# Optimization experiments

Hardware: AMD Instinct MI355X
Metric: run time of the kernel (lower is better)

Reference implementation:

```python
import jax, jax.numpy as jnp
import numpy as np

# ---- module configuration (from init_kwargs) ----
NX, NV = 2048, 1024
LX = 1.0
VMAX = 6.0
DX = LX / NX
DV = 2.0 * VMAX / NV
XS = jnp.linspace(-LX / 2 + DX / 2, LX / 2 - DX / 2, NX)
VS = jnp.linspace(-VMAX + DV / 2, VMAX - DV / 2, NV)
AE, AI = 1.0, 1836.0
ZE, ZI = -1.0, 1.0
OMEGA_C_TAU = 1.0
NU_EE, NU_II = 1.0, 0.1
DT = 1e-3
T_LBO = 1.0  # LBO temperature, u = 0


def minmod(a, b):
    return jnp.where(a * b > 0, jnp.sign(a) * jnp.minimum(jnp.abs(a), jnp.abs(b)), 0.0)


def _sl(a, lo, hi, axis):
    return jax.lax.slice_in_dim(a, lo, hi, axis=axis)


def slope_limited_flux_divergence(f_pad, F, dx, axis):
    # f_pad has N+4 cells along `axis` (2 ghost cells per side). MUSCL + minmod.
    n = f_pad.shape[axis]
    d = _sl(f_pad, 1, n, axis) - _sl(f_pad, 0, n - 1, axis)          # n-1 diffs
    sigma = minmod(_sl(d, 0, n - 2, axis), _sl(d, 1, n - 1, axis))    # slopes for cells 1..n-2
    fc = _sl(f_pad, 1, n - 1, axis)                                   # cells 1..n-2
    m = n - 2
    fL = _sl(fc, 0, m - 1, axis) + 0.5 * _sl(sigma, 0, m - 1, axis)   # left interface states
    fR = _sl(fc, 1, m, axis) - 0.5 * _sl(sigma, 1, m, axis)           # right interface states
    flux = F(fL, fR)                                                  # N+1 interface fluxes
    k = flux.shape[axis]
    return (_sl(flux, 1, k, axis) - _sl(flux, 0, k - 1, axis)) / dx   # N cells


def pad_x_periodic(f):
    return jnp.concatenate([f[-2:, :], f, f[:2, :]], axis=0)


def pad_v_zero(f):
    z = jnp.zeros((f.shape[0], 2), f.dtype)
    return jnp.concatenate([z, f, z], axis=1)


def poisson_solve(rho_c):
    # dE/dx = rho_c, zero-mean E (periodic-compatible gauge)
    E = jnp.cumsum(rho_c) * DX
    return E - jnp.mean(E)


def species_rhs(f, E, A, Z):
    v = VS[None, :]
    Fx = lambda l, r: jnp.where(v > 0, l * v, r * v)                  # upwind in x
    vdfdx = slope_limited_flux_divergence(pad_x_periodic(f), Fx, DX, axis=0)
    Ec = (OMEGA_C_TAU * Z / A) * E[:, None]
    Fv = lambda l, r: jnp.where(Ec > 0, l * Ec, r * Ec)               # upwind in v
    Edfdv = slope_limited_flux_divergence(pad_v_zero(f), Fv, DV, axis=1)
    return -vdfdx - Edfdv


def vlasov_rhs(fe, fi):
    ne = jnp.sum(fe, axis=1) * DV
    ni = jnp.sum(fi, axis=1) * DV
    E = poisson_solve(ZE * ne + ZI * ni)
    return species_rhs(fe, E, AE, ZE), species_rhs(fi, E, AI, ZI)


def ssprk2(fe, fi, dt):
    re, ri = vlasov_rhs(fe, fi)
    fe1, fi1 = fe + dt * re, fi + dt * ri
    re1, ri1 = vlasov_rhs(fe1, fi1)
    return 0.5 * (fe + fe1 + dt * re1), 0.5 * (fi + fi1 + dt * ri1)


def lbo_diagonals(lam):
    # L f = lam * d/dv( v f + T df/dv ), central differences
    vm = jnp.roll(VS, 1)
    vp = jnp.roll(VS, -1)
    dl = lam * (T_LBO / DV**2 - vm / (2 * DV))
    du = lam * (T_LBO / DV**2 + vp / (2 * DV))
    d = lam * (-2.0 * T_LBO / DV**2) * jnp.ones(NV, XS.dtype)
    return dl.at[0].set(0.0), d, du.at[-1].set(0.0)


def nu_shape():
    midpt = LX / 3
    ef = LX / 6 / 10
    h0 = lambda x: 1 + jnp.exp(x / ef - midpt / ef)
    return 1.0 / (0.5 * (h0(XS) + h0(-XS)))  # [Nx]


def thomas(dl, d, du, b):
    # Thomas algorithm; dl[0]==0 and du[-1]==0 assumed.
    def fwd(carry, inp):
        cp, bp = carry
        dli, di, dui, bi = inp
        m = di - dli * cp
        cpi = dui / m
        bpi = (bi - dli * bp) / m
        return (cpi, bpi), (cpi, bpi)
    z = jnp.zeros((), b.dtype)
    _, (cp, bp) = jax.lax.scan(fwd, (z, z), (dl, d, du, b))
    def bwd(x_next, inp):
        cpi, bpi = inp
        x = bpi - cpi * x_next
        return x, x
    _, x = jax.lax.scan(bwd, z, (cp, bp), reverse=True)
    return x


def implicit_collide(f, lam, dt):
    dl, d, du = lbo_diagonals(lam)
    nu = nu_shape()
    def solve_row(nui, frow):
        return thomas(-dt * nui * dl, 1.0 - dt * nui * d, -dt * nui * du, frow)
    return jax.vmap(solve_row)(nu, f)


def setup_inputs() -> dict:
    key = jax.random.key(0)
    k1, k2 = jax.random.split(key)
    fe = jax.random.uniform(k1, (NX, NV), dtype=jnp.float32)
    fi = jax.random.uniform(k2, (NX, NV), dtype=jnp.float32)
    return {"fe": fe, "fi": fi}


def reference(fe, fi):
    fe1, fi1 = ssprk2(fe, fi, DT)
    fe2 = implicit_collide(fe1, NU_EE, DT)
    fi2 = implicit_collide(fi1, NU_II, DT)
    return jnp.stack([fe2, fi2])  # [2, Nx, Nv]
```

## Files before the change

### kernel.cpp

```cpp
#include <hip/hip_runtime.h>
#include <math.h>

#define NX 2048
#define NV 1024
static constexpr float DXf   = 1.0f / 2048.0f;
static constexpr float DVf   = 12.0f / 1024.0f;
static constexpr float DTf   = 0.001f;
static constexpr float INV_DX = 2048.0f;
static constexpr float INV_DV = 1024.0f / 12.0f;

__device__ __forceinline__ float minmod_f(float a, float b) {
    return (a * b > 0.0f) ? (a > 0.0f ? fminf(a, b) : fmaxf(a, b)) : 0.0f;
}

__device__ __forceinline__ float frcp(float x) {
    float r = __builtin_amdgcn_rcpf(x);
    return r * (2.0f - x * r);
}

__device__ __forceinline__ void rhs4(const float* __restrict__ g, int i, int j0, float Ec,
                                     float4& f0v, float4& rv) {
    const float* rowc = g + i * NV;
    const float* rm1  = g + (((i - 1) & (NX - 1)) * NV);
    const float* rm2  = g + (((i - 2) & (NX - 1)) * NV);
    const float* rp1  = g + (((i + 1) & (NX - 1)) * NV);
    const float* rp2  = g + (((i + 2) & (NX - 1)) * NV);

    float4 c   = *(const float4*)(rowc + j0);
    float4 xm1 = *(const float4*)(rm1 + j0);
    float4 xm2 = *(const float4*)(rm2 + j0);
    float4 xp1 = *(const float4*)(rp1 + j0);
    float4 xp2 = *(const float4*)(rp2 + j0);
    float4 lm = make_float4(0.f, 0.f, 0.f, 0.f);
    float4 rp = make_float4(0.f, 0.f, 0.f, 0.f);
    if (j0 >= 4)      lm = *(const float4*)(rowc + j0 - 4);
    if (j0 <= NV - 8) rp = *(const float4*)(rowc + j0 + 4);

    float vals[8] = {lm.z, lm.w, c.x, c.y, c.z, c.w, rp.x, rp.y};
    const float* cc   = (const float*)&c;
    const float* am1  = (const float*)&xm1;
    const float* am2  = (const float*)&xm2;
    const float* ap1  = (const float*)&xp1;
    const float* ap2  = (const float*)&xp2;
    float* f0o = (float*)&f0v;
    float* ro  = (float*)&rv;

    #pragma unroll
    for (int k = 0; k < 4; ++k) {
        float f0  = cc[k];
        float fm1 = am1[k], fm2 = am2[k], fp1 = ap1[k], fp2 = ap2[k];

        float v = DVf * ((float)(j0 + k) + 0.5f) - 6.0f;
        float dm1 = fm1 - fm2, d0 = f0 - fm1, dp1 = fp1 - f0, dp2 = fp2 - fp1;
        float sm1 = minmod_f(dm1, d0);
        float s0  = minmod_f(d0, dp1);
        float sp1 = minmod_f(dp1, dp2);
        float PhiM, PhiP;
        if (v > 0.0f) {
            PhiM = (fm1 + 0.5f * sm1) * v;
            PhiP = (f0  + 0.5f * s0 ) * v;
        } else {
            PhiM = (f0  - 0.5f * s0 ) * v;
            PhiP = (fp1 - 0.5f * sp1) * v;
        }
        float vdfdx = (PhiP - PhiM) * INV_DX;

        float gm2 = vals[k], gm1 = vals[k + 1], gp1 = vals[k + 3], gp2 = vals[k + 4];
        float em1 = gm1 - gm2, e0 = f0 - gm1, ep1 = gp1 - f0, ep2 = gp2 - gp1;
        float tm1 = minmod_f(em1, e0);
        float t0  = minmod_f(e0, ep1);
        float tp1 = minmod_f(ep1, ep2);
        float GM, GP;
        if (Ec > 0.0f) {
            GM = (gm1 + 0.5f * tm1) * Ec;
            GP = (f0  + 0.5f * t0 ) * Ec;
        } else {
            GM = (f0  - 0.5f * t0 ) * Ec;
            GP = (gp1 - 0.5f * tp1) * Ec;
        }
        float Edfdv = (GP - GM) * INV_DV;

        f0o[k] = f0;
        ro[k]  = -vdfdx - Edfdv;
    }
}

__device__ __forceinline__ float compute_E(const float* __restrict__ se,
                                           const float* __restrict__ si, int i) {
    int t = threadIdx.x;
    float pref = 0.0f, wtot = 0.0f;
    #pragma unroll
    for (int q = 0; q < NX / 256; ++q) {
        int k = q * 256 + t;
        float rho = DVf * (si[k] - se[k]);
        if (k <= i) pref += rho;
        wtot += rho * (float)(NX - k);
    }
    #pragma unroll
    for (int off = 32; off > 0; off >>= 1) {
        pref += __shfl_down(pref, off, 64);
        wtot += __shfl_down(wtot, off, 64);
    }
    __shared__ float sp_[4], sw_[4];
    int lane = t & 63, wave = t >> 6;
    if (lane == 0) { sp_[wave] = pref; sw_[wave] = wtot; }
    __syncthreads();
    float P = sp_[0] + sp_[1] + sp_[2] + sp_[3];
    float W = sw_[0] + sw_[1] + sw_[2] + sw_[3];
    return DXf * (P - W * (1.0f / (float)NX));
}

__global__ __launch_bounds__(256) void moments_kernel(const float* __restrict__ fe,
                                                      const float* __restrict__ fi,
                                                      float* __restrict__ se,
                                                      float* __restrict__ si) {
    int i = blockIdx.x;
    int t = threadIdx.x;
    float4 a4 = *(const float4*)(fe + (size_t)i * NV + 4 * t);
    float4 b4 = *(const float4*)(fi + (size_t)i * NV + 4 * t);
    float a = a4.x + a4.y + a4.z + a4.w;
    float b = b4.x + b4.y + b4.z + b4.w;
    __shared__ float r1[4], r2[4];
    #pragma unroll
    for (int off = 32; off > 0; off >>= 1) {
        a += __shfl_down(a, off, 64);
        b += __shfl_down(b, off, 64);
    }
    int lane = t & 63, wave = t >> 6;
    if (lane == 0) { r1[wave] = a; r2[wave] = b; }
    __syncthreads();
    if (t == 0) {
        se[i] = r1[0] + r1[1] + r1[2] + r1[3];
        si[i] = r2[0] + r2[1] + r2[2] + r2[3];
    }
}

__global__ __launch_bounds__(256) void stage1_kernel(const float* __restrict__ fe,
                                                     const float* __restrict__ fi,
                                                     const float* __restrict__ se,
                                                     const float* __restrict__ si,
                                                     float* __restrict__ fe1,
                                                     float* __restrict__ fi1,
                                                     float* __restrict__ se1,
                                                     float* __restrict__ si1) {
    int i  = blockIdx.x;
    int sp = blockIdx.y;
    const float* g = sp ? fi : fe;
    float* out = sp ? fi1 : fe1;
    float zoa = sp ? (1.0f / 1836.0f) : -1.0f;
    float Ec = zoa * compute_E(se, si, i);
    int t = threadIdx.x;
    int j0 = 4 * t;

    float4 f0v, rv;
    rhs4(g, i, j0, Ec, f0v, rv);
    float4 o;
    o.x = f0v.x + DTf * rv.x;
    o.y = f0v.y + DTf * rv.y;
    o.z = f0v.z + DTf * rv.z;
    o.w = f0v.w + DTf * rv.w;
    *(float4*)(out + i * NV + j0) = o;

    float x = o.x + o.y + o.z + o.w;
    #pragma unroll
    for (int off = 32; off > 0; off >>= 1) x += __shfl_down(x, off, 64);
    __shared__ float sred[4];
    int lane = t & 63, wave = t >> 6;
    if (lane == 0) sred[wave] = x;
    __syncthreads();
    if (t == 0) { (sp ? si1 : se1)[i] = sred[0] + sred[1] + sred[2] + sred[3]; }
}

__global__ __launch_bounds__(256) void stage2_collide_kernel(const float* __restrict__ fe,
                                                             const float* __restrict__ fi,
                                                             const float* __restrict__ fe1,
                                                             const float* __restrict__ fi1,
                                                             const float* __restrict__ se1,
                                                             const float* __restrict__ si1,
                                                             float* __restrict__ out) {
    const float Tdv2   = 1.0f / (DVf * DVf);
    const float inv2dv = 0.5f / DVf;

    int i  = blockIdx.x;
    int sp = blockIdx.y;
    const float* h = sp ? fi : fe;
    const float* g = sp ? fi1 : fe1;
    float* orow = out + ((size_t)sp * NX + i) * NV;
    float zoa = sp ? (1.0f / 1836.0f) : -1.0f;
    float lam = sp ? 0.1f : 1.0f;
    float Ec = zoa * compute_E(se1, si1, i);
    int t = threadIdx.x;
    int lane = t & 63;
    int wave = t >> 6;

    __shared__ float lds_f[NV + NV / 16];

    {
        int j0 = 4 * t;
        float4 f0v, rv;
        rhs4(g, i, j0, Ec, f0v, rv);
        float4 h4 = *(const float4*)(h + i * NV + j0);
        int a = j0 + (j0 >> 4);
        lds_f[a]     = 0.5f * h4.x + 0.5f * f0v.x + (0.5f * DTf) * rv.x;
        lds_f[a + 1] = 0.5f * h4.y + 0.5f * f0v.y + (0.5f * DTf) * rv.y;
        lds_f[a + 2] = 0.5f * h4.z + 0.5f * f0v.z + (0.5f * DTf) * rv.z;
        lds_f[a + 3] = 0.5f * h4.w + 0.5f * f0v.w + (0.5f * DTf) * rv.w;
    }
    __syncthreads();
    if (wave != 0) return;

    float xi = DXf * ((float)i + 0.5f) - 0.5f;
    float nu = 1.0f / (1.0f + 0.5f * (expf(60.0f * xi - 20.0f) + expf(-60.0f * xi - 20.0f)));
    float K = DTf * nu * lam;
    float b = 1.0f + 2.0f * K * Tdv2;

    float Dv[16], Av[16], Cv[16];
    int j0 = lane * 16;
    int base = 17 * lane;
    #pragma unroll
    for (int r = 0; r < 16; ++r) {
        int j = j0 + r;
        float d = lds_f[base + r];
        float a = (j == 0)      ? 0.0f : -K * (Tdv2 - (DVf * ((float)j - 0.5f) - 6.0f) * inv2dv);
        float c = (j == NV - 1) ? 0.0f : -K * (Tdv2 + (DVf * ((float)j + 1.5f) - 6.0f) * inv2dv);
        if (r == 0) {
            float e = frcp(b);
            Dv[0] = e * d;
            Av[0] = e * a;
            Cv[0] = e * c;
        } else {
            float e = frcp(b - a * Cv[r - 1]);
            Dv[r] = e * (d - a * Dv[r - 1]);
            Av[r] = -e * a * Av[r - 1];
            Cv[r] = e * c;
        }
    }
    #pragma unroll
    for (int r = 14; r >= 0; --r) {
        Dv[r] = Dv[r] - Cv[r] * Dv[r + 1];
        Av[r] = Av[r] - Cv[r] * Av[r + 1];
        Cv[r] = -Cv[r] * Cv[r + 1];
    }

    float la = Av[0],  ra = Cv[0],  d0 = Dv[0];
    float lb = Av[15], rb = Cv[15], d1 = Dv[15];

    #pragma unroll
    for (int s = 1; s < 64; s <<= 1) {
        float lb_m = __shfl_up(lb, s, 64);
        float rb_m = __shfl_up(rb, s, 64);
        float d1_m = __shfl_up(d1, s, 64);
        if (lane < s) { lb_m = 0.0f; rb_m = 0.0f; d1_m = 0.0f; }
        float la_p = __shfl_down(la, s, 64);
        float ra_p = __shfl_down(ra, s, 64);
        float d0_p = __shfl_down(d0, s, 64);
        if (lane + s > 63) { la_p = 0.0f; ra_p = 0.0f; d0_p = 0.0f; }

        float m00 = 1.0f - la * rb_m;
        float m01 = -ra * la_p;
        float m10 = -lb * rb_m;
        float m11 = 1.0f - rb * la_p;
        float idet = frcp(m00 * m11 - m01 * m10);

        float Lr0 = -la * lb_m, Lr1 = -lb * lb_m;
        float Rr0 = -ra * ra_p, Rr1 = -rb * ra_p;
        float e0 = d0 - la * d1_m - ra * d0_p;
        float e1 = d1 - lb * d1_m - rb * d0_p;

        la = idet * (m11 * Lr0 - m01 * Lr1);
        lb = idet * (m00 * Lr1 - m10 * Lr0);
        ra = idet * (m11 * Rr0 - m01 * Rr1);
        rb = idet * (m00 * Rr1 - m10 * Rr0);
        d0 = idet * (m11 * e0 - m01 * e1);
        d1 = idet * (m00 * e1 - m10 * e0);
    }
    float zl = __shfl_up(d1, 1, 64);
    if (lane == 0) zl = 0.0f;
    float yr = __shfl_down(d0, 1, 64);
    if (lane == 63) yr = 0.0f;

    float x[16];
    #pragma unroll
    for (int r = 0; r < 16; ++r) x[r] = Dv[r] - Av[r] * zl - Cv[r] * yr;
    #pragma unroll
    for (int q = 0; q < 4; ++q) {
        float4 o;
        o.x = x[4 * q];
        o.y = x[4 * q + 1];
        o.z = x[4 * q + 2];
        o.w = x[4 * q + 3];
        *(float4*)(orow + j0 + 4 * q) = o;
    }
}

extern "C" void kernel_launch(void* const* d_in, const int* in_sizes, int n_in,
                              void* d_out, int out_size, void* d_ws, size_t ws_size,
                              hipStream_t stream) {
    const float* fe = (const float*)d_in[0];
    const float* fi = (const float*)d_in[1];
    float* out = (float*)d_out;
    const size_t P = (size_t)NX * NV;

    float* fe1 = (float*)d_ws;
    float* fi1 = fe1 + P;
    float* se  = fi1 + P;
    float* si  = se + NX;
    float* se1 = si + NX;
    float* si1 = se1 + NX;

    dim3 rgrid(NX, 2);

    moments_kernel<<<NX, 256, 0, stream>>>(fe, fi, se, si);
    stage1_kernel<<<rgrid, 256, 0, stream>>>(fe, fi, se, si, fe1, fi1, se1, si1);
    stage2_collide_kernel<<<rgrid, 256, 0, stream>>>(fe, fi, fe1, fi1, se1, si1, out);
}
```

Baseline: 113.6 us.

## Fuse three stage kernels into one cooperative persistent kernel with grid syncs

Replaces the moments, stage1 and stage2/collide kernels with a single cooperative kernel that uses grid.sync between phases. Each block now handles four rows, one row per wavefront, and shares one E-field prefix computation across them with a per-wave correction. The collision solve now runs on all four waves instead of one, keeping each row's data in registers rather than staging it through LDS. This removes launch overhead and idle waves, at the cost of grid-wide barriers and a grid size capped by occupancy.

Result: slower. 311.9 us (+174.6%).

```diff
diff --git a/kernel.cpp b/kernel.cpp
--- a/kernel.cpp
+++ b/kernel.cpp
@@ -1,11 +1,16 @@
 #include <hip/hip_runtime.h>
+#include <hip/hip_cooperative_groups.h>
 #include <math.h>
+
+namespace cg = cooperative_groups;
 
 #define NX 2048
 #define NV 1024
-static constexpr float DXf   = 1.0f / 2048.0f;
-static constexpr float DVf   = 12.0f / 1024.0f;
-static constexpr float DTf   = 0.001f;
+#define NGRP 1024
+
+static constexpr float DXf    = 1.0f / 2048.0f;
+static constexpr float DVf    = 12.0f / 1024.0f;
+static constexpr float DTf    = 0.001f;
 static constexpr float INV_DX = 2048.0f;
 static constexpr float INV_DV = 1024.0f / 12.0f;
 
@@ -85,15 +90,18 @@
     }
 }
 
-__device__ __forceinline__ float compute_E(const float* __restrict__ se,
-                                           const float* __restrict__ si, int i) {
+__device__ __forceinline__ float block_E(const float* __restrict__ se_,
+                                         const float* __restrict__ si_,
+                                         int r0, int wv) {
     int t = threadIdx.x;
+    __syncthreads();
+    int i3 = r0 + 3;
     float pref = 0.0f, wtot = 0.0f;
     #pragma unroll
     for (int q = 0; q < NX / 256; ++q) {
         int k = q * 256 + t;
-        float rho = DVf * (si[k] - se[k]);
-        if (k <= i) pref += rho;
+        float rho = DVf * (si_[k] - se_[k]);
+        if (k <= i3) pref += rho;
         wtot += rho * (float)(NX - k);
     }
     #pragma unroll
@@ -105,191 +113,174 @@
     int lane = t & 63, wave = t >> 6;
     if (lane == 0) { sp_[wave] = pref; sw_[wave] = wtot; }
     __syncthreads();
-    float P = sp_[0] + sp_[1] + sp_[2] + sp_[3];
-    float W = sw_[0] + sw_[1] + sw_[2] + sw_[3];
-    return DXf * (P - W * (1.0f / (float)NX));
-}
-
-__global__ __launch_bounds__(256) void moments_kernel(const float* __restrict__ fe,
-                                                      const float* __restrict__ fi,
-                                                      float* __restrict__ se,
-                                                      float* __restrict__ si) {
-    int i = blockIdx.x;
-    int t = threadIdx.x;
-    float4 a4 = *(const float4*)(fe + (size_t)i * NV + 4 * t);
-    float4 b4 = *(const float4*)(fi + (size_t)i * NV + 4 * t);
-    float a = a4.x + a4.y + a4.z + a4.w;
-    float b = b4.x + b4.y + b4.z + b4.w;
-    __shared__ float r1[4], r2[4];
-    #pragma unroll
-    for (int off = 32; off > 0; off >>= 1) {
-        a += __shfl_down(a, off, 64);
-        b += __shfl_down(b, off, 64);
-    }
-    int lane = t & 63, wave = t >> 6;
-    if (lane == 0) { r1[wave] = a; r2[wave] = b; }
-    __syncthreads();
-    if (t == 0) {
-        se[i] = r1[0] + r1[1] + r1[2] + r1[3];
-        si[i] = r2[0] + r2[1] + r2[2] + r2[3];
-    }
-}
-
-__global__ __launch_bounds__(256) void stage1_kernel(const float* __restrict__ fe,
-                                                     const float* __restrict__ fi,
-                                                     const float* __restrict__ se,
-                                                     const float* __restrict__ si,
-                                                     float* __restrict__ fe1,
-                                                     float* __restrict__ fi1,
-                                                     float* __restrict__ se1,
-                                                     float* __restrict__ si1) {
-    int i  = blockIdx.x;
-    int sp = blockIdx.y;
-    const float* g = sp ? fi : fe;
-    float* out = sp ? fi1 : fe1;
-    float zoa = sp ? (1.0f / 1836.0f) : -1.0f;
-    float Ec = zoa * compute_E(se, si, i);
-    int t = threadIdx.x;
-    int j0 = 4 * t;
-
-    float4 f0v, rv;
-    rhs4(g, i, j0, Ec, f0v, rv);
-    float4 o;
-    o.x = f0v.x + DTf * rv.x;
-    o.y = f0v.y + DTf * rv.y;
-    o.z = f0v.z + DTf * rv.z;
-    o.w = f0v.w + DTf * rv.w;
-    *(float4*)(out + i * NV + j0) = o;
-
-    float x = o.x + o.y + o.z + o.w;
-    #pragma unroll
-    for (int off = 32; off > 0; off >>= 1) x += __shfl_down(x, off, 64);
-    __shared__ float sred[4];
-    int lane = t & 63, wave = t >> 6;
-    if (lane == 0) sred[wave] = x;
-    __syncthreads();
-    if (t == 0) { (sp ? si1 : se1)[i] = sred[0] + sred[1] + sred[2] + sred[3]; }
-}
-
-__global__ __launch_bounds__(256) void stage2_collide_kernel(const float* __restrict__ fe,
-                                                             const float* __restrict__ fi,
-                                                             const float* __restrict__ fe1,
-                                                             const float* __restrict__ fi1,
-                                                             const float* __restrict__ se1,
-                                                             const float* __restrict__ si1,
-                                                             float* __restrict__ out) {
-    const float Tdv2   = 1.0f / (DVf * DVf);
-    const float inv2dv = 0.5f / DVf;
-
-    int i  = blockIdx.x;
-    int sp = blockIdx.y;
-    const float* h = sp ? fi : fe;
-    const float* g = sp ? fi1 : fe1;
-    float* orow = out + ((size_t)sp * NX + i) * NV;
-    float zoa = sp ? (1.0f / 1836.0f) : -1.0f;
-    float lam = sp ? 0.1f : 1.0f;
-    float Ec = zoa * compute_E(se1, si1, i);
-    int t = threadIdx.x;
-    int lane = t & 63;
-    int wave = t >> 6;
-
-    __shared__ float lds_f[NV + NV / 16];
-
-    {
-        int j0 = 4 * t;
-        float4 f0v, rv;
-        rhs4(g, i, j0, Ec, f0v, rv);
-        float4 h4 = *(const float4*)(h + i * NV + j0);
-        int a = j0 + (j0 >> 4);
-        lds_f[a]     = 0.5f * h4.x + 0.5f * f0v.x + (0.5f * DTf) * rv.x;
-        lds_f[a + 1] = 0.5f * h4.y + 0.5f * f0v.y + (0.5f * DTf) * rv.y;
-        lds_f[a + 2] = 0.5f * h4.z + 0.5f * f0v.z + (0.5f * DTf) * rv.z;
-        lds_f[a + 3] = 0.5f * h4.w + 0.5f * f0v.w + (0.5f * DTf) * rv.w;
-    }
-    __syncthreads();
-    if (wave != 0) return;
-
-    float xi = DXf * ((float)i + 0.5f) - 0.5f;
-    float nu = 1.0f / (1.0f + 0.5f * (expf(60.0f * xi - 20.0f) + expf(-60.0f * xi - 20.0f)));
-    float K = DTf * nu * lam;
-    float b = 1.0f + 2.0f * K * Tdv2;
-
-    float Dv[16], Av[16], Cv[16];
-    int j0 = lane * 16;
-    int base = 17 * lane;
-    #pragma unroll
-    for (int r = 0; r < 16; ++r) {
-        int j = j0 + r;
-        float d = lds_f[base + r];
-        float a = (j == 0)      ? 0.0f : -K * (Tdv2 - (DVf * ((float)j - 0.5f) - 6.0f) * inv2dv);
-        float c = (j == NV - 1) ? 0.0f : -K * (Tdv2 + (DVf * ((float)j + 1.5f) - 6.0f) * inv2dv);
-        if (r == 0) {
-            float e = frcp(b);
-            Dv[0] = e * d;
-            Av[0] = e * a;
-            Cv[0] = e * c;
-        } else {
-            float e = frcp(b - a * Cv[r - 1]);
-            Dv[r] = e * (d - a * Dv[r - 1]);
-            Av[r] = -e * a * Av[r - 1];
-            Cv[r] = e * c;
-        }
-    }
-    #pragma unroll
-    for (int r = 14; r >= 0; --r) {
-        Dv[r] = Dv[r] - Cv[r] * Dv[r + 1];
-        Av[r] = Av[r] - Cv[r] * Av[r + 1];
-        Cv[r] = -Cv[r] * Cv[r + 1];
-    }
-
-    float la = Av[0],  ra = Cv[0],  d0 = Dv[0];
-    float lb = Av[15], rb = Cv[15], d1 = Dv[15];
-
-    #pragma unroll
-    for (int s = 1; s < 64; s <<= 1) {
-        float lb_m = __shfl_up(lb, s, 64);
-        float rb_m = __shfl_up(rb, s, 64);
-        float d1_m = __shfl_up(d1, s, 64);
-        if (lane < s) { lb_m = 0.0f; rb_m = 0.0f; d1_m = 0.0f; }
-        float la_p = __shfl_down(la, s, 64);
-        float ra_p = __shfl_down(ra, s, 64);
-        float d0_p = __shfl_down(d0, s, 64);
-        if (lane + s > 63) { la_p = 0.0f; ra_p = 0.0f; d0_p = 0.0f; }
-
-        float m00 = 1.0f - la * rb_m;
-        float m01 = -ra * la_p;
-        float m10 = -lb * rb_m;
-        float m11 = 1.0f - rb * la_p;
-        float idet = frcp(m00 * m11 - m01 * m10);
-
-        float Lr0 = -la * lb_m, Lr1 = -lb * lb_m;
-        float Rr0 = -ra * ra_p, Rr1 = -rb * ra_p;
-        float e0 = d0 - la * d1_m - ra * d0_p;
-        float e1 = d1 - lb * d1_m - rb * d0_p;
-
-        la = idet * (m11 * Lr0 - m01 * Lr1);
-        lb = idet * (m00 * Lr1 - m10 * Lr0);
-        ra = idet * (m11 * Rr0 - m01 * Rr1);
-        rb = idet * (m00 * Rr1 - m10 * Rr0);
-        d0 = idet * (m11 * e0 - m01 * e1);
-        d1 = idet * (m00 * e1 - m10 * e0);
-    }
-    float zl = __shfl_up(d1, 1, 64);
-    if (lane == 0) zl = 0.0f;
-    float yr = __shfl_down(d0, 1, 64);
-    if (lane == 63) yr = 0.0f;
-
-    float x[16];
-    #pragma unroll
-    for (int r = 0; r < 16; ++r) x[r] = Dv[r] - Av[r] * zl - Cv[r] * yr;
-    #pragma unroll
-    for (int q = 0; q < 4; ++q) {
-        float4 o;
-        o.x = x[4 * q];
-        o.y = x[4 * q + 1];
-        o.z = x[4 * q + 2];
-        o.w = x[4 * q + 3];
-        *(float4*)(orow + j0 + 4 * q) = o;
+    float P3 = sp_[0] + sp_[1] + sp_[2] + sp_[3];
+    float W  = sw_[0] + sw_[1] + sw_[2] + sw_[3];
+    float rho1 = DVf * (si_[r0 + 1] - se_[r0 + 1]);
+    float rho2 = DVf * (si_[r0 + 2] - se_[r0 + 2]);
+    float rho3 = DVf * (si_[r0 + 3] - se_[r0 + 3]);
+    float corr = (wv == 3) ? 0.0f
+               : (wv == 2) ? rho3
+               : (wv == 1) ? (rho3 + rho2)
+                           : (rho3 + rho2 + rho1);
+    return DXf * (P3 - corr - W * (1.0f / (float)NX));
+}
+
+__global__ __launch_bounds__(256, 4) void fused_kernel(
+    const float* __restrict__ fe, const float* __restrict__ fi,
+    float* __restrict__ fe1, float* __restrict__ fi1,
+    float* __restrict__ se,  float* __restrict__ si,
+    float* __restrict__ se1, float* __restrict__ si1,
+    float* __restrict__ out)
+{
+    cg::grid_group grid = cg::this_grid();
+    const int t = threadIdx.x, lane = t & 63, wv = t >> 6;
+
+    for (int g = blockIdx.x; g < NGRP; g += gridDim.x) {
+        const int sp = g >> 9, r0 = (g & 511) << 2;
+        const float* f = sp ? fi : fe;
+        const int row = r0 + wv;
+        const float* rp = f + row * NV;
+        float s = 0.0f;
+        #pragma unroll
+        for (int q = 0; q < 4; ++q) {
+            float4 a = *(const float4*)(rp + 4 * lane + 256 * q);
+            s += a.x + a.y + a.z + a.w;
+        }
+        #pragma unroll
+        for (int off = 32; off > 0; off >>= 1) s += __shfl_down(s, off, 64);
+        if (lane == 0) (sp ? si : se)[row] = s;
+    }
+    grid.sync();
+
+    for (int g = blockIdx.x; g < NGRP; g += gridDim.x) {
+        const int sp = g >> 9, r0 = (g & 511) << 2;
+        const float* f = sp ? fi : fe;
+        float* f1 = sp ? fi1 : fe1;
+        const float zoa = sp ? (1.0f / 1836.0f) : -1.0f;
+        const float Ec = zoa * block_E(se, si, r0, wv);
+        const int row = r0 + wv;
+        float s = 0.0f;
+        #pragma unroll
+        for (int q = 0; q < 4; ++q) {
+            const int j0 = 4 * lane + 256 * q;
+            float4 f0v, rv;
+            rhs4(f, row, j0, Ec, f0v, rv);
+            float4 o;
+            o.x = f0v.x + DTf * rv.x;
+            o.y = f0v.y + DTf * rv.y;
+            o.z = f0v.z + DTf * rv.z;
+            o.w = f0v.w + DTf * rv.w;
+            *(float4*)(f1 + row * NV + j0) = o;
+            s += o.x + o.y + o.z + o.w;
+        }
+        #pragma unroll
+        for (int off = 32; off > 0; off >>= 1) s += __shfl_down(s, off, 64);
+        if (lane == 0) (sp ? si1 : se1)[row] = s;
+    }
+    grid.sync();
+
+    for (int g = blockIdx.x; g < NGRP; g += gridDim.x) {
+        const int sp = g >> 9, r0 = (g & 511) << 2;
+        const float* h  = sp ? fi : fe;
+        const float* f1 = sp ? fi1 : fe1;
+        const float zoa = sp ? (1.0f / 1836.0f) : -1.0f;
+        const float lam = sp ? 0.1f : 1.0f;
+        const float Ec = zoa * block_E(se1, si1, r0, wv);
+        const int row = r0 + wv;
+        float* orow = out + ((size_t)sp * NX + row) * NV;
+
+        const float Tdv2   = 1.0f / (DVf * DVf);
+        const float inv2dv = 0.5f / DVf;
+        const float xi = DXf * ((float)row + 0.5f) - 0.5f;
+        const float nu = 1.0f / (1.0f + 0.5f * (expf(60.0f * xi - 20.0f) + expf(-60.0f * xi - 20.0f)));
+        const float K = DTf * nu * lam;
+        const float b = 1.0f + 2.0f * K * Tdv2;
+
+        const int j0 = 16 * lane;
+        float d[16];
+        #pragma unroll
+        for (int q = 0; q < 4; ++q) {
+            float4 f0v, rv;
+            rhs4(f1, row, j0 + 4 * q, Ec, f0v, rv);
+            float4 h4 = *(const float4*)(h + row * NV + j0 + 4 * q);
+            d[4 * q + 0] = 0.5f * h4.x + 0.5f * f0v.x + (0.5f * DTf) * rv.x;
+            d[4 * q + 1] = 0.5f * h4.y + 0.5f * f0v.y + (0.5f * DTf) * rv.y;
+            d[4 * q + 2] = 0.5f * h4.z + 0.5f * f0v.z + (0.5f * DTf) * rv.z;
+            d[4 * q + 3] = 0.5f * h4.w + 0.5f * f0v.w + (0.5f * DTf) * rv.w;
+        }
+
+        float Dv[16], Av[16], Cv[16];
+        #pragma unroll
+        for (int r = 0; r < 16; ++r) {
+            int j = j0 + r;
+            float a = (j == 0)      ? 0.0f : -K * (Tdv2 - (DVf * ((float)j - 0.5f) - 6.0f) * inv2dv);
+            float c = (j == NV - 1) ? 0.0f : -K * (Tdv2 + (DVf * ((float)j + 1.5f) - 6.0f) * inv2dv);
+            if (r == 0) {
+                float e = frcp(b);
+                Dv[0] = e * d[0];
+                Av[0] = e * a;
+                Cv[0] = e * c;
+            } else {
+                float e = frcp(b - a * Cv[r - 1]);
+                Dv[r] = e * (d[r] - a * Dv[r - 1]);
+                Av[r] = -e * a * Av[r - 1];
+                Cv[r] = e * c;
+            }
+        }
+        #pragma unroll
+        for (int r = 14; r >= 0; --r) {
+            Dv[r] = Dv[r] - Cv[r] * Dv[r + 1];
+            Av[r] = Av[r] - Cv[r] * Av[r + 1];
+            Cv[r] = -Cv[r] * Cv[r + 1];
+        }
+
+        float la = Av[0],  ra = Cv[0],  d0 = Dv[0];
+        float lb = Av[15], rb = Cv[15], d1 = Dv[15];
+        #pragma unroll
+        for (int s = 1; s < 64; s <<= 1) {
+            float lb_m = __shfl_up(lb, s, 64);
+            float rb_m = __shfl_up(rb, s, 64);
+            float d1_m = __shfl_up(d1, s, 64);
+            if (lane < s) { lb_m = 0.0f; rb_m = 0.0f; d1_m = 0.0f; }
+            float la_p = __shfl_down(la, s, 64);
+            float ra_p = __shfl_down(ra, s, 64);
+            float d0_p = __shfl_down(d0, s, 64);
+            if (lane + s > 63) { la_p = 0.0f; ra_p = 0.0f; d0_p = 0.0f; }
+
+            float m00 = 1.0f - la * rb_m;
+            float m01 = -ra * la_p;
+            float m10 = -lb * rb_m;
+            float m11 = 1.0f - rb * la_p;
+            float idet = frcp(m00 * m11 - m01 * m10);
+
+            float Lr0 = -la * lb_m, Lr1 = -lb * lb_m;
+            float Rr0 = -ra * ra_p, Rr1 = -rb * ra_p;
+            float e0 = d0 - la * d1_m - ra * d0_p;
+            float e1 = d1 - lb * d1_m - rb * d0_p;
+
+            la = idet * (m11 * Lr0 - m01 * Lr1);
+            lb = idet * (m00 * Lr1 - m10 * Lr0);
+            ra = idet * (m11 * Rr0 - m01 * Rr1);
+            rb = idet * (m00 * Rr1 - m10 * Rr0);
+            d0 = idet * (m11 * e0 - m01 * e1);
+            d1 = idet * (m00 * e1 - m10 * e0);
+        }
+        float zl = __shfl_up(d1, 1, 64);
+        if (lane == 0) zl = 0.0f;
+        float yr = __shfl_down(d0, 1, 64);
+        if (lane == 63) yr = 0.0f;
+
+        #pragma unroll
+        for (int r = 0; r < 16; ++r) Dv[r] = Dv[r] - Av[r] * zl - Cv[r] * yr;
+        #pragma unroll
+        for (int q = 0; q < 4; ++q) {
+            float4 o;
+            o.x = Dv[4 * q + 0];
+            o.y = Dv[4 * q + 1];
+            o.z = Dv[4 * q + 2];
+            o.w = Dv[4 * q + 3];
+            *(float4*)(orow + j0 + 4 * q) = o;
+        }
     }
 }
 
@@ -308,9 +299,23 @@
     float* se1 = si + NX;
     float* si1 = se1 + NX;
 
-    dim3 rgrid(NX, 2);
-
-    moments_kernel<<<NX, 256, 0, stream>>>(fe, fi, se, si);
-    stage1_kernel<<<rgrid, 256, 0, stream>>>(fe, fi, se, si, fe1, fi1, se1, si1);
-    stage2_collide_kernel<<<rgrid, 256, 0, stream>>>(fe, fi, fe1, fi1, se1, si1, out);
-}
+    static int g_grid = 0;
+    if (g_grid == 0) {
+        int maxb = 0;
+        if (hipOccupancyMaxActiveBlocksPerMultiprocessor(&maxb, fused_kernel, 256, 0) != hipSuccess ||
+            maxb <= 0)
+            maxb = 2;
+        int ncu = 256;
+        hipDeviceProp_t prop;
+        int dev = 0;
+        if (hipGetDevice(&dev) == hipSuccess && hipGetDeviceProperties(&prop, dev) == hipSuccess)
+            ncu = prop.multiProcessorCount;
+        long cap = (long)maxb * (long)ncu;
+        g_grid = (int)(cap < NGRP ? cap : NGRP);
+    }
+
+    void* args[] = {(void*)&fe, (void*)&fi, (void*)&fe1, (void*)&fi1,
+                    (void*)&se, (void*)&si, (void*)&se1, (void*)&si1, (void*)&out};
+    hipLaunchCooperativeKernel((const void*)fused_kernel, dim3(g_grid), dim3(256),
+                               args, 0, stream);
+}
```
